# Kernel optimization log

Measured on AMD Instinct MI355X. Metric: run time of the kernel, lower is better.

The kernel has to match this reference:

```python
import jax, jax.numpy as jnp
import numpy as np

TAU = 2.0  # LIF membrane time constant (spikingjelly default)
SCALE = 0.125

@jax.custom_vjp
def heaviside(x):
    return (x >= 0).astype(x.dtype)

def _hv_fwd(x):
    return heaviside(x), x

def _hv_bwd(x, g):
    s = jax.nn.sigmoid(4.0 * x)  # sigmoid surrogate, alpha=4
    return (g * 4.0 * s * (1.0 - s),)

heaviside.defvjp(_hv_fwd, _hv_bwd)

def lif(x, v_th):
    """Multi-step LIF over leading time axis. x: [T, ...]. decay_input, hard reset to 0."""
    def step(v, xt):
        v = v + (xt - v) / TAU
        s = heaviside(v - v_th)
        return v * (1.0 - s), s
    return jax.lax.scan(step, jnp.zeros_like(x[0]), x)[1]

def conv1x1(x, w, b=None):
    # x: [T,B,C,N], w: [O,C]
    y = jnp.einsum('oc,tbcn->tbon', w, x)
    if b is not None:
        y = y + b[None, None, :, None]
    return y

def bn(x, p, eps=1e-5):
    # inference-mode BatchNorm1d over channel axis; p: [4,C] = gamma,beta,mean,var
    g, b, m, v = p[0], p[1], p[2], p[3]
    inv = g / jnp.sqrt(v + eps)
    return x * inv[None, None, :, None] + (b - m * inv)[None, None, :, None]

def setup_inputs() -> dict:
    key = jax.random.key(0)
    ks = jax.random.split(key, 10)
    T, B, C, H, W = 4, 32, 512, 16, 16
    wscale = 1.0 / np.sqrt(C)
    def bn_params(k):
        k1, k2, k3, k4 = jax.random.split(k, 4)
        gamma = 1.0 + 0.1 * jax.random.normal(k1, (C,))
        beta = 0.1 * jax.random.normal(k2, (C,))
        mean = 0.1 * jax.random.normal(k3, (C,))
        var = 1.0 + 0.1 * jax.random.uniform(k4, (C,))
        return jnp.stack([gamma, beta, mean, var])
    return {
        'x': jax.random.normal(ks[0], (T, B, C, H, W), dtype=jnp.float32),
        'res_attn': jnp.zeros((1,), dtype=jnp.float32),
        'q_w': wscale * jax.random.normal(ks[1], (C, C), dtype=jnp.float32),
        'k_w': wscale * jax.random.normal(ks[2], (C, C), dtype=jnp.float32),
        'v_w': wscale * jax.random.normal(ks[3], (C, C), dtype=jnp.float32),
        'proj_w': wscale * jax.random.normal(ks[4], (C, C), dtype=jnp.float32),
        'proj_b': 0.01 * jax.random.normal(ks[5], (C,), dtype=jnp.float32),
        'q_bn': bn_params(ks[6]),
        'k_bn': bn_params(ks[7]),
        'v_bn': bn_params(ks[8]),
        'p_bn': bn_params(ks[9]),
    }

def reference(x, res_attn, q_w, k_w, v_w, proj_w, proj_b, q_bn, k_bn, v_bn, p_bn):
    T, B, C, H, W = x.shape
    num_heads = 8
    d = C // num_heads
    N = H * W
    xf = x.reshape(T, B, C, N)

    def branch(w, p, v_th):
        return lif(bn(conv1x1(xf, w), p), v_th)

    def to_heads(t):  # [T,B,C,N] -> [T,B,h,N,d]
        return t.transpose(0, 1, 3, 2).reshape(T, B, N, num_heads, d).transpose(0, 1, 3, 2, 4)

    q = to_heads(branch(q_w, q_bn, 1.0))
    k = to_heads(branch(k_w, k_bn, 1.0))
    v = to_heads(branch(v_w, v_bn, 1.0))

    # linear (non-softmax) attention: q @ (k^T @ v) * scale
    kv = jnp.einsum('tbhnd,tbhne->tbhde', k, v)
    a = jnp.einsum('tbhnd,tbhde->tbhne', q, kv) * SCALE  # [T,B,h,N,d]

    # [T,B,h,N,d] -> transpose(3,4) -> [T,B,h,d,N] -> [T,B,C,N]
    a = jnp.swapaxes(a, 3, 4).reshape(T, B, C, N)
    a = lif(a, 0.5)  # attn_lif with v_threshold=0.5

    out = conv1x1(a, proj_w, proj_b)
    out = bn(out, p_bn).reshape(T, B, C, H, W)
    out = lif(out, 1.0)
    return out, v
```

## Files before the change

### kernel.cpp

```cpp
#include <hip/hip_runtime.h>
#include <stdint.h>

#define T_ 4
#define B_ 32
#define C_ 512
#define N_ 256
#define NH_ 8
#define NB_ (N_ / 8)
#define BITS_BYTES_ ((size_t)(T_ * B_ * C_) * NB_)

typedef float f32x2 __attribute__((ext_vector_type(2)));

__device__ __forceinline__ f32x2 pk_mul_d(f32x2 a, f32x2 b) {
  f32x2 r;
  asm("v_pk_mul_f32 %0, %1, %2" : "=v"(r) : "v"(a), "v"(b));
  return r;
}
__device__ __forceinline__ f32x2 pk_mul_x(f32x2 a, f32x2 b) {
  f32x2 r;
  asm("v_pk_mul_f32 %0, %1, %2 op_sel:[0,1] op_sel_hi:[1,0]"
      : "=v"(r) : "v"(a), "v"(b));
  return r;
}
__device__ __forceinline__ void pk_add_acc(f32x2& acc, f32x2 p) {
  asm("v_pk_add_f32 %0, %0, %1" : "+v"(acc) : "v"(p));
}
__device__ __forceinline__ void pk_fma_d(f32x2& acc, f32x2 a, f32x2 b) {
  asm("v_pk_fma_f32 %0, %1, %2, %0" : "+v"(acc) : "v"(a), "v"(b));
}
__device__ __forceinline__ void pk_fma_x(f32x2& acc, f32x2 a, f32x2 b) {
  asm("v_pk_fma_f32 %0, %1, %2, %0 op_sel:[0,1,0] op_sel_hi:[1,0,1]"
      : "+v"(acc) : "v"(a), "v"(b));
}

__device__ __forceinline__ void gload_lds16(const void* g, void* l) {
  __builtin_amdgcn_global_load_lds(
      (const __attribute__((address_space(1))) unsigned int*)g,
      (__attribute__((address_space(3))) unsigned int*)l, 16, 0, 0);
}


__global__ __launch_bounds__(256, 2) void qkv_gemm_lif(
    const float* __restrict__ x, const float* __restrict__ wq,
    const float* __restrict__ wk, const float* __restrict__ wv,
    const float* __restrict__ bnq, const float* __restrict__ bnk,
    const float* __restrict__ bnv,
    uint8_t* __restrict__ sbits, float* __restrict__ out1) {
#pragma clang fp contract(off)
  const int bx = blockIdx.x;
  const int br = bx >> 4;
  const int tile = bx & 15;
  const int b  = blockIdx.y;
  const int ot = tile >> 1, nt = tile & 1;
  const float* w = (br == 0) ? wq : (br == 1) ? wk : wv;
  const float* bn = (br == 0) ? bnq : (br == 1) ? bnk : bnv;
  uint8_t* sb = sbits + (size_t)br * BITS_BYTES_;

  const int tid = threadIdx.x;
  const int tx = tid & 15, ty = tid >> 4;
  const int o0 = ot * 64, n0 = nt * 128;

  __shared__ float As[32][64];
  __shared__ float Bs[32][128];

  float inv[4], add[4];
#pragma unroll
  for (int i = 0; i < 4; ++i) {
    int o = o0 + ty * 4 + i;
    float g = bn[o], be = bn[C_ + o], mm = bn[2 * C_ + o], va = bn[3 * C_ + o];
    float iv = g / sqrtf(va + 1e-5f);
    inv[i] = iv;
    add[i] = be - mm * iv;
  }

  float vst[4][8];
#pragma unroll
  for (int i = 0; i < 4; ++i)
#pragma unroll
    for (int j = 0; j < 8; ++j) vst[i][j] = 0.f;

  const int sa_o = tid & 63, sa_k8 = (tid >> 6) * 8;
  const int wv_ = tid >> 6;

  for (int t = 0; t < T_; ++t) {
    const float* xb = x + (size_t)(t * B_ + b) * (C_ * N_);
    f32x2 acc_d[2][4], acc_x[2][4];
#pragma unroll
    for (int ip = 0; ip < 2; ++ip)
#pragma unroll
      for (int jp = 0; jp < 4; ++jp) {
        acc_d[ip][jp] = (f32x2){0.f, 0.f};
        acc_x[ip][jp] = (f32x2){0.f, 0.f};
      }

    for (int kc = 0; kc < C_; kc += 32) {
      const float* wrow = w + (size_t)(o0 + sa_o) * C_ + kc + sa_k8;
      float4 a0 = *(const float4*)(wrow);
      float4 a1 = *(const float4*)(wrow + 4);
      __syncthreads();
#pragma unroll
      for (int r = 0; r < 4; ++r) {
        int slot0 = r * 256 + wv_ * 64;
        int slot = slot0 + (tid & 63);
        int row = slot >> 5, col = (slot & 31) * 4;
        gload_lds16(xb + (size_t)(kc + row) * N_ + n0 + col,
                    (char*)&Bs[0][0] + (size_t)slot0 * 16);
      }
      As[sa_k8 + 0][sa_o] = a0.x; As[sa_k8 + 1][sa_o] = a0.y;
      As[sa_k8 + 2][sa_o] = a0.z; As[sa_k8 + 3][sa_o] = a0.w;
      As[sa_k8 + 4][sa_o] = a1.x; As[sa_k8 + 5][sa_o] = a1.y;
      As[sa_k8 + 6][sa_o] = a1.z; As[sa_k8 + 7][sa_o] = a1.w;
      __syncthreads();
#pragma unroll
      for (int k = 0; k < 32; ++k) {
        float4 av4 = *(const float4*)(&As[k][ty * 4]);
        float4 bq0 = *(const float4*)(&Bs[k][tx * 4]);
        float4 bq1 = *(const float4*)(&Bs[k][64 + tx * 4]);
        f32x2 a2[2] = {(f32x2){av4.x, av4.y}, (f32x2){av4.z, av4.w}};
        f32x2 b2[4] = {(f32x2){bq0.x, bq0.y}, (f32x2){bq0.z, bq0.w},
                       (f32x2){bq1.x, bq1.y}, (f32x2){bq1.z, bq1.w}};
#pragma unroll
        for (int ip = 0; ip < 2; ++ip)
#pragma unroll
          for (int jp = 0; jp < 4; ++jp) {
            f32x2 pd = pk_mul_d(a2[ip], b2[jp]);
            f32x2 px = pk_mul_x(a2[ip], b2[jp]);
            pk_add_acc(acc_d[ip][jp], pd);
            pk_add_acc(acc_x[ip][jp], px);
          }
      }
    }

    {
      size_t tb = (size_t)(t * B_ + b);
      unsigned nibsA = 0, nibsB = 0;
#pragma unroll
      for (int i = 0; i < 4; ++i) {
#pragma unroll
        for (int jj = 0; jj < 8; ++jj) {
          int ip = i >> 1, il = i & 1, jp = jj >> 1, jl = jj & 1;
          float a = (il == jl) ? acc_d[ip][jp][il] : acc_x[ip][jp][il];
          float y0 = a * inv[i];
          float y = y0 + add[i];
          float d = y - vst[i][jj];
          float vs = vst[i][jj] + d * 0.5f;
          unsigned sp = (vs >= 1.0f) ? 1u : 0u;
          vst[i][jj] = sp ? 0.f : vs;
          if (jj < 4) nibsA |= sp << (4 * i + jj);
          else        nibsB |= sp << (4 * i + jj - 4);
        }
      }
      unsigned oA = __shfl_xor(nibsA, 1);
      unsigned oB = __shfl_xor(nibsB, 1);
      int m = tx >> 1;
      if ((tx & 1) == 0) {
#pragma unroll
        for (int i = 0; i < 4; ++i) {
          int o = o0 + ty * 4 + i;
          unsigned byte_ = ((nibsA >> (4 * i)) & 0xF) | (((oA >> (4 * i)) & 0xF) << 4);
          sb[(tb * C_ + o) * NB_ + (n0 >> 3) + m] = (uint8_t)byte_;
        }
      } else {
#pragma unroll
        for (int i = 0; i < 4; ++i) {
          int o = o0 + ty * 4 + i;
          unsigned byte_ = ((oB >> (4 * i)) & 0xF) | (((nibsB >> (4 * i)) & 0xF) << 4);
          sb[(tb * C_ + o) * NB_ + (n0 >> 3) + 8 + m] = (uint8_t)byte_;
        }
      }
      if (br == 2) {
#pragma unroll
        for (int i = 0; i < 4; ++i) {
          int o = o0 + ty * 4 + i;
          int h = o >> 6, dd = o & 63;
          size_t base = ((tb * NH_ + h) * (size_t)N_) * 64 + dd;
#pragma unroll
          for (int jj = 0; jj < 8; ++jj) {
            int n = n0 + ((jj < 4) ? (tx * 4 + jj) : (64 + tx * 4 + jj - 4));
            unsigned sp = (jj < 4) ? ((nibsA >> (4 * i + jj)) & 1u)
                                   : ((nibsB >> (4 * i + jj - 4)) & 1u);
            out1[base + (size_t)n * 64] = sp ? 1.0f : 0.0f;
          }
        }
      }
    }
  }
}

__global__ __launch_bounds__(512, 1) void attn_lif(
    const uint8_t* __restrict__ bits, uint8_t* __restrict__ abits) {
#pragma clang fp contract(off)
  const unsigned long long* qb = (const unsigned long long*)bits;
  const unsigned long long* kb = qb + BITS_BYTES_ / 8;
  const unsigned long long* vb = kb + BITS_BYTES_ / 8;
  unsigned long long* ap = (unsigned long long*)abits;

  const int h = blockIdx.x, b = blockIdx.y;
  const int tid = threadIdx.x;
  const int lane = tid & 63, wave = tid >> 6;
  const int nw = wave & 3, eh = wave >> 2;

  __shared__ unsigned long long kbl[64][4];
  __shared__ unsigned long long vbl[64][4];
  __shared__ float kvl[64][64];

  float state[32];
#pragma unroll
  for (int e = 0; e < 32; ++e) state[e] = 0.f;

  for (int t = 0; t < T_; ++t) {
    size_t row0 = (size_t)(t * B_ + b) * C_ + h * 64;
    {
      int i = tid & 255, c = i >> 2, w = i & 3;
      if (tid < 256) kbl[c][w] = kb[(row0 + c) * 4 + w];
      else           vbl[c][w] = vb[(row0 + c) * 4 + w];
    }
    __syncthreads();
    {
      int d = tid & 63, eb = (tid >> 6) * 8;
#pragma unroll
      for (int e2 = 0; e2 < 8; ++e2) {
        int e = eb + e2;
        int s = 0;
#pragma unroll
        for (int w = 0; w < 4; ++w) s += __popcll(kbl[d][w] & vbl[e][w]);
        kvl[d][e] = (float)s;
      }
    }
    __syncthreads();
    float acc[32];
#pragma unroll
    for (int e = 0; e < 32; ++e) acc[e] = 0.f;
    for (int d = 0; d < 64; ++d) {
      unsigned long long qw = qb[(row0 + d) * 4 + nw];
      float qf = (float)(unsigned)((qw >> lane) & 1ULL);
      const float* kr = &kvl[d][eh * 32];
#pragma unroll
      for (int e = 0; e < 32; ++e) acc[e] = acc[e] + qf * kr[e];
    }
    {
#pragma unroll
      for (int e2 = 0; e2 < 32; ++e2) {
        int e = eh * 32 + e2;
        float a = acc[e2] * 0.125f;
        float d0 = a - state[e2];
        float vs = state[e2] + d0 * 0.5f;
        int sp = (vs >= 0.5f) ? 1 : 0;
        state[e2] = sp ? 0.f : vs;
        unsigned long long m = __ballot(sp);
        if (lane == 0) ap[(row0 + e) * 4 + nw] = m;
      }
    }
    __syncthreads();
  }
}

__global__ __launch_bounds__(256, 2) void proj_gemm_lif(
    const uint8_t* __restrict__ ab, const float* __restrict__ wp,
    const float* __restrict__ pb, const float* __restrict__ bnp,
    float* __restrict__ out0) {
  const int b = blockIdx.y;
  const int ot = blockIdx.x >> 1, nt = blockIdx.x & 1;
  const int tid = threadIdx.x;
  const int tx = tid & 15, ty = tid >> 4;
  const int o0 = ot * 64, n0 = nt * 128;

  __shared__ float As[2][16][64];
  __shared__ float Bs[2][16][128];

  float inv[4], add[4], bias[4];
  {
#pragma clang fp contract(off)
#pragma unroll
    for (int i = 0; i < 4; ++i) {
      int o = o0 + ty * 4 + i;
      float g = bnp[o], be = bnp[C_ + o], mm = bnp[2 * C_ + o], va = bnp[3 * C_ + o];
      float iv = g / sqrtf(va + 1e-5f);
      inv[i] = iv;
      add[i] = be - mm * iv;
      bias[i] = pb[o];
    }
  }

  float vst[4][8];
#pragma unroll
  for (int i = 0; i < 4; ++i)
#pragma unroll
    for (int j = 0; j < 8; ++j) vst[i][j] = 0.f;

  const int sa_o = tid & 63, sa_kq = (tid >> 6) * 4;
  const int br_ = tid >> 4, bq16 = tid & 15;

  for (int t = 0; t < T_; ++t) {
    f32x2 acc_d[2][4], acc_x[2][4];
#pragma unroll
    for (int ip = 0; ip < 2; ++ip)
#pragma unroll
      for (int jp = 0; jp < 4; ++jp) {
        acc_d[ip][jp] = (f32x2){0.f, 0.f};
        acc_x[ip][jp] = (f32x2){0.f, 0.f};
      }
    size_t tb = (size_t)(t * B_ + b);

    {
      float4 a4 = *(const float4*)(wp + (size_t)(o0 + sa_o) * C_ + 0 + sa_kq);
      uint8_t by = ab[(tb * C_ + 0 + br_) * NB_ + (n0 >> 3) + bq16];
      __syncthreads();
      As[0][sa_kq + 0][sa_o] = a4.x; As[0][sa_kq + 1][sa_o] = a4.y;
      As[0][sa_kq + 2][sa_o] = a4.z; As[0][sa_kq + 3][sa_o] = a4.w;
      int nb = bq16 * 8;
#pragma unroll
      for (int j = 0; j < 8; ++j) Bs[0][br_][nb + j] = (float)((by >> j) & 1);
      __syncthreads();
    }

    for (int it = 0; it < 32; ++it) {
      const int cur = it & 1;
      float4 a4; uint8_t by = 0;
      if (it < 31) {
        int kc = (it + 1) * 16;
        a4 = *(const float4*)(wp + (size_t)(o0 + sa_o) * C_ + kc + sa_kq);
        by = ab[(tb * C_ + kc + br_) * NB_ + (n0 >> 3) + bq16];
      }
#pragma unroll
      for (int k = 0; k < 16; ++k) {
        float4 av4 = *(const float4*)(&As[cur][k][ty * 4]);
        float4 bq0 = *(const float4*)(&Bs[cur][k][tx * 4]);
        float4 bq1 = *(const float4*)(&Bs[cur][k][64 + tx * 4]);
        f32x2 a2[2] = {(f32x2){av4.x, av4.y}, (f32x2){av4.z, av4.w}};
        f32x2 b2[4] = {(f32x2){bq0.x, bq0.y}, (f32x2){bq0.z, bq0.w},
                       (f32x2){bq1.x, bq1.y}, (f32x2){bq1.z, bq1.w}};
#pragma unroll
        for (int ip = 0; ip < 2; ++ip)
#pragma unroll
          for (int jp = 0; jp < 4; ++jp) {
            pk_fma_d(acc_d[ip][jp], a2[ip], b2[jp]);
            pk_fma_x(acc_x[ip][jp], a2[ip], b2[jp]);
          }
      }
      if (it < 31) {
        const int nxt = cur ^ 1;
        As[nxt][sa_kq + 0][sa_o] = a4.x; As[nxt][sa_kq + 1][sa_o] = a4.y;
        As[nxt][sa_kq + 2][sa_o] = a4.z; As[nxt][sa_kq + 3][sa_o] = a4.w;
        int nb = bq16 * 8;
#pragma unroll
        for (int j = 0; j < 8; ++j) Bs[nxt][br_][nb + j] = (float)((by >> j) & 1);
        __syncthreads();
      }
    }

    {
#pragma clang fp contract(off)
#pragma unroll
      for (int i = 0; i < 4; ++i) {
        int o = o0 + ty * 4 + i;
        float4 r0, r1;
#pragma unroll
        for (int jj = 0; jj < 8; ++jj) {
          int ip = i >> 1, il = i & 1, jp = jj >> 1, jl = jj & 1;
          float a = (il == jl) ? acc_d[ip][jp][il] : acc_x[ip][jp][il];
          float y1 = a + bias[i];
          float y2 = y1 * inv[i];
          float y = y2 + add[i];
          float d0 = y - vst[i][jj];
          float vs = vst[i][jj] + d0 * 0.5f;
          int sp = (vs >= 1.0f) ? 1 : 0;
          vst[i][jj] = sp ? 0.f : vs;
          if (jj < 4) (&r0.x)[jj] = sp ? 1.0f : 0.0f;
          else        (&r1.x)[jj - 4] = sp ? 1.0f : 0.0f;
        }
        float* dst = out0 + (tb * C_ + o) * N_ + n0;
        *(float4*)(dst + tx * 4) = r0;
        *(float4*)(dst + 64 + tx * 4) = r1;
      }
    }
  }
}


extern "C" void kernel_launch(void* const* d_in, const int* in_sizes, int n_in,
                              void* d_out, int out_size, void* d_ws, size_t ws_size,
                              hipStream_t stream) {
  const float* x   = (const float*)d_in[0];
  const float* qw  = (const float*)d_in[2];
  const float* kw  = (const float*)d_in[3];
  const float* vw  = (const float*)d_in[4];
  const float* pw  = (const float*)d_in[5];
  const float* pbb = (const float*)d_in[6];
  const float* qbn = (const float*)d_in[7];
  const float* kbn = (const float*)d_in[8];
  const float* vbn = (const float*)d_in[9];
  const float* pbn = (const float*)d_in[10];

  uint8_t* bits  = (uint8_t*)d_ws;
  uint8_t* abits = bits + 3 * BITS_BYTES_;

  float* out0 = (float*)d_out;
  float* out1 = out0 + (size_t)T_ * B_ * C_ * N_;

  qkv_gemm_lif<<<dim3(48, 32), dim3(256), 0, stream>>>(
      x, qw, kw, vw, qbn, kbn, vbn, bits, out1);
  attn_lif<<<dim3(8, 32), dim3(512), 0, stream>>>(bits, abits);
  proj_gemm_lif<<<dim3(16, 32), dim3(256), 0, stream>>>(abits, pw, pbb, pbn,
                                                        out0);
}
```

Measured before the change: 1.240 ms.

## Pre-transpose QKV weights and double-buffer GEMM tiles via direct LDS loads

Adds a small kernel that transposes the three QKV weight matrices into workspace on every call, so the GEMM can stage weight tiles with async global-to-LDS loads instead of register loads followed by scattered LDS stores. The QKV GEMM main loop now double-buffers its A and B LDS tiles, prefetching the next K chunk while computing the current one and using one barrier per iteration. The aim is to hide global load latency and cut LDS store overhead. In exchange it adds an extra kernel launch and a weight transpose pass, doubles shared memory per block (which may reduce occupancy), and moves the spike bit buffers to an offset in workspace.

```diff
diff --git a/kernel.cpp b/kernel.cpp
--- a/kernel.cpp
+++ b/kernel.cpp
@@ -40,9 +40,23 @@
 }
 
 
+__global__ __launch_bounds__(256) void transpose_w(
+    const float* __restrict__ wq, const float* __restrict__ wk,
+    const float* __restrict__ wv, float* __restrict__ wt_all) {
+  const float* src = (blockIdx.z == 0) ? wq : (blockIdx.z == 1) ? wk : wv;
+  float* dst = wt_all + (size_t)blockIdx.z * C_ * C_;
+  __shared__ float tile[32][33];
+  int bx = blockIdx.x * 32, by = blockIdx.y * 32;
+  int tx = threadIdx.x, ty = threadIdx.y;
+#pragma unroll
+  for (int i = ty; i < 32; i += 8) tile[i][tx] = src[(size_t)(by + i) * C_ + bx + tx];
+  __syncthreads();
+#pragma unroll
+  for (int i = ty; i < 32; i += 8) dst[(size_t)(bx + i) * C_ + by + tx] = tile[tx][i];
+}
+
 __global__ __launch_bounds__(256, 2) void qkv_gemm_lif(
-    const float* __restrict__ x, const float* __restrict__ wq,
-    const float* __restrict__ wk, const float* __restrict__ wv,
+    const float* __restrict__ x, const float* __restrict__ wt_all,
     const float* __restrict__ bnq, const float* __restrict__ bnk,
     const float* __restrict__ bnv,
     uint8_t* __restrict__ sbits, float* __restrict__ out1) {
@@ -52,7 +66,7 @@
   const int tile = bx & 15;
   const int b  = blockIdx.y;
   const int ot = tile >> 1, nt = tile & 1;
-  const float* w = (br == 0) ? wq : (br == 1) ? wk : wv;
+  const float* wt = wt_all + (size_t)br * C_ * C_;
   const float* bn = (br == 0) ? bnq : (br == 1) ? bnk : bnv;
   uint8_t* sb = sbits + (size_t)br * BITS_BYTES_;
 
@@ -60,8 +74,8 @@
   const int tx = tid & 15, ty = tid >> 4;
   const int o0 = ot * 64, n0 = nt * 128;
 
-  __shared__ float As[32][64];
-  __shared__ float Bs[32][128];
+  __shared__ float As[2][32][64];
+  __shared__ float Bs[2][32][128];
 
   float inv[4], add[4];
 #pragma unroll
@@ -79,11 +93,31 @@
 #pragma unroll
     for (int j = 0; j < 8; ++j) vst[i][j] = 0.f;
 
-  const int sa_o = tid & 63, sa_k8 = (tid >> 6) * 8;
   const int wv_ = tid >> 6;
+  const int lane = tid & 63;
 
   for (int t = 0; t < T_; ++t) {
     const float* xb = x + (size_t)(t * B_ + b) * (C_ * N_);
+
+    auto stage = [&](int buf, int kc) {
+#pragma unroll
+      for (int r = 0; r < 2; ++r) {
+        int slot0 = r * 256 + wv_ * 64;
+        int slot = slot0 + lane;
+        int row = slot >> 4, col = (slot & 15) * 4;
+        gload_lds16(wt + (size_t)(kc + row) * C_ + o0 + col,
+                    (char*)&As[buf][0][0] + (size_t)slot0 * 16);
+      }
+#pragma unroll
+      for (int r = 0; r < 4; ++r) {
+        int slot0 = r * 256 + wv_ * 64;
+        int slot = slot0 + lane;
+        int row = slot >> 5, col = (slot & 31) * 4;
+        gload_lds16(xb + (size_t)(kc + row) * N_ + n0 + col,
+                    (char*)&Bs[buf][0][0] + (size_t)slot0 * 16);
+      }
+    };
+
     f32x2 acc_d[2][4], acc_x[2][4];
 #pragma unroll
     for (int ip = 0; ip < 2; ++ip)
@@ -93,29 +127,17 @@
         acc_x[ip][jp] = (f32x2){0.f, 0.f};
       }
 
-    for (int kc = 0; kc < C_; kc += 32) {
-      const float* wrow = w + (size_t)(o0 + sa_o) * C_ + kc + sa_k8;
-      float4 a0 = *(const float4*)(wrow);
-      float4 a1 = *(const float4*)(wrow + 4);
-      __syncthreads();
-#pragma unroll
-      for (int r = 0; r < 4; ++r) {
-        int slot0 = r * 256 + wv_ * 64;
-        int slot = slot0 + (tid & 63);
-        int row = slot >> 5, col = (slot & 31) * 4;
-        gload_lds16(xb + (size_t)(kc + row) * N_ + n0 + col,
-                    (char*)&Bs[0][0] + (size_t)slot0 * 16);
-      }
-      As[sa_k8 + 0][sa_o] = a0.x; As[sa_k8 + 1][sa_o] = a0.y;
-      As[sa_k8 + 2][sa_o] = a0.z; As[sa_k8 + 3][sa_o] = a0.w;
-      As[sa_k8 + 4][sa_o] = a1.x; As[sa_k8 + 5][sa_o] = a1.y;
-      As[sa_k8 + 6][sa_o] = a1.z; As[sa_k8 + 7][sa_o] = a1.w;
-      __syncthreads();
+    stage(0, 0);
+    __syncthreads();
+
+    for (int it = 0; it < 16; ++it) {
+      const int cur = it & 1;
+      if (it < 15) stage(cur ^ 1, (it + 1) * 32);
 #pragma unroll
       for (int k = 0; k < 32; ++k) {
-        float4 av4 = *(const float4*)(&As[k][ty * 4]);
-        float4 bq0 = *(const float4*)(&Bs[k][tx * 4]);
-        float4 bq1 = *(const float4*)(&Bs[k][64 + tx * 4]);
+        float4 av4 = *(const float4*)(&As[cur][k][ty * 4]);
+        float4 bq0 = *(const float4*)(&Bs[cur][k][tx * 4]);
+        float4 bq1 = *(const float4*)(&Bs[cur][k][64 + tx * 4]);
         f32x2 a2[2] = {(f32x2){av4.x, av4.y}, (f32x2){av4.z, av4.w}};
         f32x2 b2[4] = {(f32x2){bq0.x, bq0.y}, (f32x2){bq0.z, bq0.w},
                        (f32x2){bq1.x, bq1.y}, (f32x2){bq1.z, bq1.w}};
@@ -129,6 +151,7 @@
             pk_add_acc(acc_x[ip][jp], px);
           }
       }
+      __syncthreads();
     }
 
     {
@@ -392,14 +415,16 @@
   const float* vbn = (const float*)d_in[9];
   const float* pbn = (const float*)d_in[10];
 
-  uint8_t* bits  = (uint8_t*)d_ws;
+  float* wt = (float*)d_ws;
+  uint8_t* bits  = (uint8_t*)d_ws + 3u * 1024u * 1024u;
   uint8_t* abits = bits + 3 * BITS_BYTES_;
 
   float* out0 = (float*)d_out;
   float* out1 = out0 + (size_t)T_ * B_ * C_ * N_;
 
+  transpose_w<<<dim3(16, 16, 3), dim3(32, 8), 0, stream>>>(qw, kw, vw, wt);
   qkv_gemm_lif<<<dim3(48, 32), dim3(256), 0, stream>>>(
-      x, qw, kw, vw, qbn, kbn, vbn, bits, out1);
+      x, wt, qbn, kbn, vbn, bits, out1);
   attn_lif<<<dim3(8, 32), dim3(512), 0, stream>>>(bits, abits);
   proj_gemm_lif<<<dim3(16, 32), dim3(256), 0, stream>>>(abits, pw, pbb, pbn,
                                                         out0);
```

New measurement: 1.275 ms. 1.03x slower.
